# Kernel tuning notes

Hardware: AMD Instinct MI355X
Metric: run time of the kernel (lower is better)

Reference implementation:

```python
import jax, jax.numpy as jnp
from jax import lax
import numpy as np

TAU = 10.0      # tauSr == tauRef
THR = 1.0       # theta
WIDTH = 1.0     # tauRho (surrogate width)
SCALE = 1.0     # scaleRho (surrogate scale)
DECAY = float(np.exp(-1.0 / TAU))


@jax.custom_vjp
def _heaviside(v):
    # spike = 1[v >= theta]
    return (v >= THR).astype(v.dtype)

def _heaviside_fwd(v):
    return _heaviside(v), v

def _heaviside_bwd(v, g):
    # SLAYER exponential surrogate pdf: scaleRho/tauRho * exp(-|v-theta|/tauRho)
    return (g * (SCALE / WIDTH) * jnp.exp(-jnp.abs(v - THR) / WIDTH),)

_heaviside.defvjp(_heaviside_fwd, _heaviside_bwd)


def _conv2d(x, w, pad):
    # x: (B, Cin, H, W), w: (Cout, Cin, kh, kw); SLAYER convs have no bias
    return lax.conv_general_dilated(
        x, w, window_strides=(1, 1), padding=[(pad, pad), (pad, pad)],
        dimension_numbers=("NCHW", "OIHW", "NCHW"))


def _sumpool(x, k):
    # SLAYER pool = sum over kxk window (times a learned scalar applied outside)
    B, C, H, W = x.shape
    return x.reshape(B, C, H // k, k, W // k, k).sum(axis=(3, 5))


def _psp(seq):
    # exponential synaptic (PSP) filter along time: s[t] = a*s[t-1] + x[t]
    a = jnp.asarray(DECAY, seq.dtype)
    def step(s, x_t):
        s = a * s + x_t
        return s, s
    _, out = lax.scan(step, jnp.zeros_like(seq[0]), seq)
    return out  # (T, ...)


def _spikes(u):
    # thresholded spiking with decaying refractory feedback (scaleRef=1):
    # v[t] = u[t] - r[t]; s[t] = 1[v >= theta]; r[t+1] = b*(r[t] + theta*s[t])
    b = jnp.asarray(DECAY, u.dtype)
    def step(r, u_t):
        s = _heaviside(u_t - r)
        r_next = b * (r + THR * s)
        return r_next, s
    _, out = lax.scan(step, jnp.zeros_like(u[0]), u)
    return out  # (T, ...)


def _forward(x, conv1_w, conv2_w, lin_w, w_pool1, w_pool2):
    N, T, C, H, W = x.shape  # (64, 100, 2, 32, 32)
    h = _conv2d(x.reshape(N * T, C, H, W), conv1_w, 2)        # (NT, 4, 32, 32)
    h = _sumpool(h, 4) * w_pool1                               # (NT, 4, 8, 8)
    h = h.reshape(N, T, 4, 8, 8).swapaxes(0, 1)                # (T, N, 4, 8, 8)
    s1 = _spikes(_psp(h))                                      # (T, N, 4, 8, 8)
    h2 = _conv2d(s1.reshape(T * N, 4, 8, 8), conv2_w, 1)       # (TN, 8, 8, 8)
    h2 = (_sumpool(h2, 2) * w_pool2).reshape(T, N, 8, 4, 4)    # (T, N, 8, 4, 4)
    s2 = _spikes(_psp(h2))                                     # (T, N, 8, 4, 4)
    # dense = full-spatial conv (2, 8, 4, 4) -> (N, T, 2)
    return jnp.einsum("tnchw,ochw->nto", s2, lin_w)


def setup_inputs() -> dict:
    key = jax.random.key(0)
    ks = jax.random.split(key, 4)
    x = (jax.random.uniform(ks[0], (64, 100, 2, 32, 32)) < 0.1).astype(jnp.float32)
    conv1_w = jax.random.normal(ks[1], (4, 2, 5, 5), jnp.float32) * 0.3
    conv2_w = jax.random.normal(ks[2], (8, 4, 3, 3), jnp.float32) * 0.3
    lin_w = jax.random.normal(ks[3], (2, 8, 4, 4), jnp.float32) * 0.3
    w_pool1 = jnp.float32(1.0 / 16.0)  # 1.1*theta / (16 * 1.1)
    w_pool2 = jnp.float32(1.0 / 4.0)   # 1.1*theta / (4 * 1.1)
    return {"x": x, "conv1_w": conv1_w, "conv2_w": conv2_w, "lin_w": lin_w,
            "w_pool1": w_pool1, "w_pool2": w_pool2}


def reference(x, conv1_w, conv2_w, lin_w, w_pool1, w_pool2):
    return _forward(x, conv1_w, conv2_w, lin_w, w_pool1, w_pool2)
```

## Files before the change

### kernel.cpp

```cpp
#include <hip/hip_runtime.h>


#define DECAY 0.9048374180359595f

#define BAR_LGKM() asm volatile("s_waitcnt lgkmcnt(0)\n\ts_barrier" ::: "memory")
#define FENCE_LGKM() asm volatile("s_waitcnt lgkmcnt(0)" ::: "memory")

__global__ __launch_bounds__(128) void k0_fold(const float* __restrict__ w1,
        const float* __restrict__ w2, const float* __restrict__ wp1,
        const float* __restrict__ wp2, float* __restrict__ wl1,
        float* __restrict__ wl2, float* __restrict__ out) {
    const int tid = threadIdx.x;
    out[blockIdx.x * 128 + tid] = 0.f;
    if (blockIdx.x != 0) return;
    const float p1 = wp1[0], p2 = wp2[0];
    for (int idx = tid; idx < 512; idx += 128) {
        const int f = idx & 7, c = (idx >> 3) & 3, e = (idx >> 5) & 7, cin = idx >> 8;
        const int cc = c * 2 + cin;
        int alo = e - 3; if (alo < 0) alo = 0;
        int ahi = e;     if (ahi > 4) ahi = 4;
        int blo = f - 3; if (blo < 0) blo = 0;
        int bhi = f;     if (bhi > 4) bhi = 4;
        float s = 0.f;
        for (int a = alo; a <= ahi; ++a)
            for (int b = blo; b <= bhi; ++b)
                s += w1[cc * 25 + a * 5 + b];
        wl1[(cin * 8 + e) * 32 + c * 8 + f] = s * p1;
    }
    for (int idx = tid; idx < 512; idx += 128) {
        const int c2 = idx & 7, f = (idx >> 3) & 3, e = (idx >> 5) & 3, cin = idx >> 7;
        int alo = e - 1; if (alo < 0) alo = 0;
        int ahi = e;     if (ahi > 2) ahi = 2;
        int blo = f - 1; if (blo < 0) blo = 0;
        int bhi = f;     if (bhi > 2) bhi = 2;
        float s = 0.f;
        for (int aa = alo; aa <= ahi; ++aa)
            for (int bb = blo; bb <= bhi; ++bb)
                s += w2[((c2 * 4 + cin) * 3 + aa) * 3 + bb];
        wl2[c2 * 68 + cin * 16 + e * 4 + f] = s * p2;
    }
}

__global__ __launch_bounds__(64) void k1(const float* __restrict__ x,
        const float* __restrict__ wg, float* __restrict__ u1) {
    __shared__ __align__(16) float xs[2 * 1296];
    __shared__ __align__(16) float wl[512];
    const int lane = threadIdx.x;
    const int frame = blockIdx.x;
    const int n = frame / 100, t = frame % 100;

    *(float4*)(wl + 4 * lane)       = *(const float4*)(wg + 4 * lane);
    *(float4*)(wl + 256 + 4 * lane) = *(const float4*)(wg + 256 + 4 * lane);

    #pragma unroll
    for (int m0 = 0; m0 < 128; m0 += 64) {
        const int m = m0 + lane;
        if (m < 72) {
            const int cin = m / 36, rem = m % 36;
            const int rr = rem / 9, q4 = rem % 9;
            const int pr = (rr == 0) ? 0 : (rr == 1) ? 9 : (rr == 2) ? 26 : 35;
            *(float4*)(xs + cin * 1296 + pr * 36 + q4 * 4) = make_float4(0.f, 0.f, 0.f, 0.f);
        }
    }
    #pragma unroll
    for (int m0 = 0; m0 < 192; m0 += 64) {
        const int m = m0 + lane;
        if (m < 144) {
            const int cin = m / 72, rem = m % 72;
            const int side = rem & 1, pr = rem >> 1;
            *(float2*)(xs + cin * 1296 + pr * 36 + side * 34) = make_float2(0.f, 0.f);
        }
    }
    const float4* xg = (const float4*)(x + (size_t)frame * 2048);
    #pragma unroll
    for (int q = 0; q < 8; ++q) {
        const int m = q * 64 + lane;
        const float4 v = xg[m];
        const int li = 4 * m;
        const int cin = li >> 10, row = (li >> 5) & 31, col = li & 31;
        const int r = row + 2;
        const int pr = (r & 3) * 9 + (r >> 2);
        float* d = xs + cin * 1296 + pr * 36 + col + 2;
        *(float2*)(d)     = make_float2(v.x, v.y);
        *(float2*)(d + 2) = make_float2(v.z, v.w);
    }
    FENCE_LGKM();

    const int cp = lane >> 5;
    const int i  = (lane >> 2) & 7;
    const int jh = (lane >> 1) & 1;
    const int eh = lane & 1;

    float acc[2][4] = {{0.f, 0.f, 0.f, 0.f}, {0.f, 0.f, 0.f, 0.f}};
    const float* tb = xs + (i + eh) * 36 + jh * 16;
    #pragma unroll
    for (int cin = 0; cin < 2; ++cin) {
        #pragma unroll
        for (int et = 0; et < 4; ++et) {
            const int ro = cin * 1296 + et * 9 * 36;
            float xr[20];
            #pragma unroll
            for (int b = 0; b < 5; ++b)
                *(float4*)(xr + 4 * b) = *(const float4*)(tb + ro + 4 * b);
            float wv[16];
            const float* wp = wl + (cin * 8 + eh * 4 + et) * 32 + cp * 16;
            #pragma unroll
            for (int q = 0; q < 4; ++q)
                *(float4*)(wv + 4 * q) = *(const float4*)(wp + 4 * q);
            #pragma unroll
            for (int cl = 0; cl < 2; ++cl) {
                #pragma unroll
                for (int jj = 0; jj < 4; ++jj) {
                    const int o = 4 * jj;
                    acc[cl][jj] += xr[o]*wv[cl*8]     + xr[o+1]*wv[cl*8+1]
                                 + xr[o+2]*wv[cl*8+2] + xr[o+3]*wv[cl*8+3]
                                 + xr[o+4]*wv[cl*8+4] + xr[o+5]*wv[cl*8+5]
                                 + xr[o+6]*wv[cl*8+6] + xr[o+7]*wv[cl*8+7];
                }
            }
        }
    }
    #pragma unroll
    for (int cl = 0; cl < 2; ++cl)
        #pragma unroll
        for (int jj = 0; jj < 4; ++jj)
            acc[cl][jj] += __shfl_xor(acc[cl][jj], 1);

    const float o0 = eh ? acc[1][0] : acc[0][0];
    const float o1 = eh ? acc[1][1] : acc[0][1];
    const float o2 = eh ? acc[1][2] : acc[0][2];
    const float o3 = eh ? acc[1][3] : acc[0][3];
    *(float4*)(u1 + (size_t)t * 16384 + n * 256 + (2 * cp + eh) * 64 + i * 8 + jh * 4) =
        make_float4(o0, o1, o2, o3);
}

__global__ __launch_bounds__(256) void kf(const float* __restrict__ u1,
        const float* __restrict__ wl2g, const float* __restrict__ lw,
        float* __restrict__ out) {
    __shared__ __align__(16) float ls1[32 * 660];
    __shared__ __align__(16) float ls2[32 * 36];
    const int tid = threadIdx.x;
    const int n = blockIdx.x >> 2, qtr = blockIdx.x & 3;
    const int wave = tid >> 6, l64 = tid & 63;
    const float a = DECAY;

    for (int m = tid; m < 5280; m += 256)
        *(float4*)(ls1 + 4 * m) = make_float4(0.f, 0.f, 0.f, 0.f);

    const int cs = tid >> 6, rowi = (tid >> 3) & 7, col = tid & 7;
    const int pr1 = (((rowi + 1) & 1) * 5) + ((rowi + 1) >> 1);
    const int woff = cs * 160 + pr1 * 16 + 1 + col;
    const float* up = u1 + n * 256 + tid;

    const int sub = tid >> 4, l16 = tid & 15;
    const int c2l = l16 >> 3, i2 = (l16 >> 1) & 3, jhp = l16 & 1;
    const int c2g = qtr * 2 + c2l;

    float4 wreg[16];
    {
        const float* wbase = wl2g + c2g * 68;
        #pragma unroll
        for (int q = 0; q < 16; ++q)
            wreg[q] = *(const float4*)(wbase + (q >> 2) * 16 + (q & 3) * 4);
    }

    float dwA[8], dwB[8];
    {
        const int idx = l64 & 3;
        #pragma unroll
        for (int m = 0; m < 8; ++m) {
            dwA[m] = lw[qtr * 32 + idx * 8 + m];
            dwB[m] = lw[128 + qtr * 32 + idx * 8 + m];
        }
    }

    float psp = 0.f, rr = 0.f;
    float psp2 = 0.f, rr2 = 0.f;

    float vbuf[32];
    #pragma unroll
    for (int k = 0; k < 32; ++k) vbuf[k] = up[(size_t)k * 16384];

    BAR_LGKM();

    #pragma unroll 1
    for (int rd = 0; rd < 4; ++rd) {
        const int t0 = rd * 32;
        const int cnt = (rd == 3) ? 4 : 32;

        float sreg[32];
        #pragma unroll
        for (int k = 0; k < 32; ++k) {
            if (k < cnt) {
                psp = a * psp + vbuf[k];
                const float vv = psp - rr;
                const float s = (vv >= 1.f) ? 1.f : 0.f;
                rr = a * (rr + s);
                sreg[k] = s;
            }
        }
        #pragma unroll
        for (int k = 0; k < 32; ++k) {
            const int tt = t0 + 32 + k;
            if (tt < 100) vbuf[k] = up[(size_t)tt * 16384];
        }
        #pragma unroll
        for (int k = 0; k < 32; ++k)
            if (k < cnt) ls1[k * 660 + woff] = sreg[k];
        BAR_LGKM();

        #pragma unroll
        for (int pass = 0; pass < 2; ++pass) {
            const int slot = sub + 16 * pass;
            if (slot < cnt) {
                const float* tb = ls1 + slot * 660 + i2 * 16 + 4 * jhp;
                float acc0 = 0.f, acc1 = 0.f;
                #pragma unroll
                for (int cin = 0; cin < 4; ++cin) {
                    #pragma unroll
                    for (int e = 0; e < 4; ++e) {
                        const int C = cin * 160 + ((e & 1) * 5 + (e >> 1)) * 16;
                        float xr[6];
                        *(float4*)(xr)     = *(const float4*)(tb + C);
                        *(float2*)(xr + 4) = *(const float2*)(tb + C + 4);
                        const float4 wf = wreg[cin * 4 + e];
                        acc0 += xr[0] * wf.x; acc0 += xr[1] * wf.y;
                        acc0 += xr[2] * wf.z; acc0 += xr[3] * wf.w;
                        acc1 += xr[2] * wf.x; acc1 += xr[3] * wf.y;
                        acc1 += xr[4] * wf.z; acc1 += xr[5] * wf.w;
                    }
                }
                *(float2*)(ls2 + slot * 36 + c2l * 16 + i2 * 4 + 2 * jhp) =
                    make_float2(acc0, acc1);
            }
        }
        BAR_LGKM();

        if (wave == 0) {
            if (l64 < 32) {
                #pragma unroll
                for (int k = 0; k < 32; ++k) {
                    if (k < cnt) {
                        const float u = ls2[k * 36 + l64];
                        psp2 = a * psp2 + u;
                        const float vv = psp2 - rr2;
                        const float s = (vv >= 1.f) ? 1.f : 0.f;
                        rr2 = a * (rr2 + s);
                        ls2[k * 36 + l64] = s;
                    }
                }
            }
            FENCE_LGKM();
            #pragma unroll
            for (int pass = 0; pass < 2; ++pass) {
                const int slot = (l64 >> 2) + 16 * pass;
                const int idx = l64 & 3;
                if (slot < cnt) {
                    float a0 = 0.f, a1 = 0.f;
                    #pragma unroll
                    for (int m = 0; m < 8; ++m) {
                        const float s = ls2[slot * 36 + idx * 8 + m];
                        a0 += s * dwA[m];
                        a1 += s * dwB[m];
                    }
                    a0 += __shfl_down(a0, 2); a0 += __shfl_down(a0, 1);
                    a1 += __shfl_down(a1, 2); a1 += __shfl_down(a1, 1);
                    if (idx == 0) {
                        const int tt = t0 + slot;
                        atomicAdd(&out[n * 200 + tt * 2],     a0);
                        atomicAdd(&out[n * 200 + tt * 2 + 1], a1);
                    }
                }
            }
        }
    }
}

extern "C" void kernel_launch(void* const* d_in, const int* in_sizes, int n_in,
                              void* d_out, int out_size, void* d_ws, size_t ws_size,
                              hipStream_t stream) {
    const float* x   = (const float*)d_in[0];
    const float* w1  = (const float*)d_in[1];
    const float* w2  = (const float*)d_in[2];
    const float* lw  = (const float*)d_in[3];
    const float* wp1 = (const float*)d_in[4];
    const float* wp2 = (const float*)d_in[5];

    float* u1  = (float*)d_ws;
    float* wl1 = u1 + 1638400;
    float* wl2 = wl1 + 512;
    float* out = (float*)d_out;

    k0_fold<<<100, 128, 0, stream>>>(w1, w2, wp1, wp2, wl1, wl2, out);
    k1<<<6400, 64, 0, stream>>>(x, wl1, u1);
    kf<<<256, 256, 0, stream>>>(u1, wl2, lw, out);
}
```

Measured before the change: 123.9 us.

## Process all 100 timesteps in one pass with unpadded spike layout in LDS

The final fused kernel now loads all 100 timesteps of conv1 output into registers up front, runs the first spiking recurrence over the whole sequence, and stores spikes into a compact unpadded LDS buffer. The 4-round chunked pipeline and its per-round barriers are gone, and conv2 handles padding with clamped row indices and selects instead of a zero-padded halo layout. This removes the zero-initialisation pass and most barriers. In exchange it uses about 118 KB of LDS and 100 live registers per thread, which can cut occupancy or cause spills, and it no longer overlaps loads with compute across rounds.

Measured after the change: 119.8 us. 3.3% less time.

```diff
diff --git a/kernel.cpp b/kernel.cpp
--- a/kernel.cpp
+++ b/kernel.cpp
@@ -137,19 +137,13 @@
 __global__ __launch_bounds__(256) void kf(const float* __restrict__ u1,
         const float* __restrict__ wl2g, const float* __restrict__ lw,
         float* __restrict__ out) {
-    __shared__ __align__(16) float ls1[32 * 660];
-    __shared__ __align__(16) float ls2[32 * 36];
+    __shared__ __align__(16) float ls1[100 * 260];
+    __shared__ __align__(16) float ls2[100 * 36];
     const int tid = threadIdx.x;
     const int n = blockIdx.x >> 2, qtr = blockIdx.x & 3;
     const int wave = tid >> 6, l64 = tid & 63;
     const float a = DECAY;
 
-    for (int m = tid; m < 5280; m += 256)
-        *(float4*)(ls1 + 4 * m) = make_float4(0.f, 0.f, 0.f, 0.f);
-
-    const int cs = tid >> 6, rowi = (tid >> 3) & 7, col = tid & 7;
-    const int pr1 = (((rowi + 1) & 1) * 5) + ((rowi + 1) >> 1);
-    const int woff = cs * 160 + pr1 * 16 + 1 + col;
     const float* up = u1 + n * 256 + tid;
 
     const int sub = tid >> 4, l16 = tid & 15;
@@ -174,102 +168,94 @@
         }
     }
 
-    float psp = 0.f, rr = 0.f;
-    float psp2 = 0.f, rr2 = 0.f;
-
-    float vbuf[32];
-    #pragma unroll
-    for (int k = 0; k < 32; ++k) vbuf[k] = up[(size_t)k * 16384];
-
+    float vbuf[100];
+    #pragma unroll
+    for (int k = 0; k < 100; ++k) vbuf[k] = up[(size_t)k * 16384];
+    {
+        float psp = 0.f, rr = 0.f;
+        #pragma unroll
+        for (int k = 0; k < 100; ++k) {
+            psp = a * psp + vbuf[k];
+            const float vv = psp - rr;
+            const float s = (vv >= 1.f) ? 1.f : 0.f;
+            rr = a * (rr + s);
+            ls1[k * 260 + tid] = s;
+        }
+    }
     BAR_LGKM();
 
     #pragma unroll 1
-    for (int rd = 0; rd < 4; ++rd) {
-        const int t0 = rd * 32;
-        const int cnt = (rd == 3) ? 4 : 32;
-
-        float sreg[32];
-        #pragma unroll
-        for (int k = 0; k < 32; ++k) {
-            if (k < cnt) {
-                psp = a * psp + vbuf[k];
-                const float vv = psp - rr;
+    for (int pass = 0; pass < 7; ++pass) {
+        const int slot = sub + 16 * pass;
+        if (slot < 100) {
+            const float* sb = ls1 + slot * 260;
+            float acc0 = 0.f, acc1 = 0.f;
+            #pragma unroll
+            for (int cin = 0; cin < 4; ++cin) {
+                #pragma unroll
+                for (int e = 0; e < 4; ++e) {
+                    const int ri = 2 * i2 + e - 1;
+                    const int rc = (ri < 0) ? 0 : (ri > 7 ? 7 : ri);
+                    const bool rok = (ri >= 0) && (ri <= 7);
+                    float rr8[8];
+                    const float* rp = sb + cin * 64 + rc * 8;
+                    *(float4*)(rr8)     = *(const float4*)(rp);
+                    *(float4*)(rr8 + 4) = *(const float4*)(rp + 4);
+                    float xr[6];
+                    xr[0] = jhp ? rr8[3] : 0.0f;
+                    xr[1] = jhp ? rr8[4] : rr8[0];
+                    xr[2] = jhp ? rr8[5] : rr8[1];
+                    xr[3] = jhp ? rr8[6] : rr8[2];
+                    xr[4] = jhp ? rr8[7] : rr8[3];
+                    xr[5] = jhp ? 0.0f   : rr8[4];
+                    if (!rok) {
+                        #pragma unroll
+                        for (int m = 0; m < 6; ++m) xr[m] = 0.0f;
+                    }
+                    const float4 wf = wreg[cin * 4 + e];
+                    acc0 += xr[0] * wf.x; acc0 += xr[1] * wf.y;
+                    acc0 += xr[2] * wf.z; acc0 += xr[3] * wf.w;
+                    acc1 += xr[2] * wf.x; acc1 += xr[3] * wf.y;
+                    acc1 += xr[4] * wf.z; acc1 += xr[5] * wf.w;
+                }
+            }
+            *(float2*)(ls2 + slot * 36 + c2l * 16 + i2 * 4 + 2 * jhp) =
+                make_float2(acc0, acc1);
+        }
+    }
+    BAR_LGKM();
+
+    if (wave == 0) {
+        if (l64 < 32) {
+            float psp2 = 0.f, rr2 = 0.f;
+            #pragma unroll
+            for (int k = 0; k < 100; ++k) {
+                const float u = ls2[k * 36 + l64];
+                psp2 = a * psp2 + u;
+                const float vv = psp2 - rr2;
                 const float s = (vv >= 1.f) ? 1.f : 0.f;
-                rr = a * (rr + s);
-                sreg[k] = s;
-            }
-        }
-        #pragma unroll
-        for (int k = 0; k < 32; ++k) {
-            const int tt = t0 + 32 + k;
-            if (tt < 100) vbuf[k] = up[(size_t)tt * 16384];
-        }
-        #pragma unroll
-        for (int k = 0; k < 32; ++k)
-            if (k < cnt) ls1[k * 660 + woff] = sreg[k];
-        BAR_LGKM();
-
-        #pragma unroll
-        for (int pass = 0; pass < 2; ++pass) {
-            const int slot = sub + 16 * pass;
-            if (slot < cnt) {
-                const float* tb = ls1 + slot * 660 + i2 * 16 + 4 * jhp;
-                float acc0 = 0.f, acc1 = 0.f;
+                rr2 = a * (rr2 + s);
+                ls2[k * 36 + l64] = s;
+            }
+        }
+        FENCE_LGKM();
+        const int idx = l64 & 3;
+        #pragma unroll 1
+        for (int pass = 0; pass < 7; ++pass) {
+            const int slot = (l64 >> 2) + 16 * pass;
+            if (slot < 100) {
+                float a0 = 0.f, a1 = 0.f;
                 #pragma unroll
-                for (int cin = 0; cin < 4; ++cin) {
-                    #pragma unroll
-                    for (int e = 0; e < 4; ++e) {
-                        const int C = cin * 160 + ((e & 1) * 5 + (e >> 1)) * 16;
-                        float xr[6];
-                        *(float4*)(xr)     = *(const float4*)(tb + C);
-                        *(float2*)(xr + 4) = *(const float2*)(tb + C + 4);
-                        const float4 wf = wreg[cin * 4 + e];
-                        acc0 += xr[0] * wf.x; acc0 += xr[1] * wf.y;
-                        acc0 += xr[2] * wf.z; acc0 += xr[3] * wf.w;
-                        acc1 += xr[2] * wf.x; acc1 += xr[3] * wf.y;
-                        acc1 += xr[4] * wf.z; acc1 += xr[5] * wf.w;
-                    }
-                }
-                *(float2*)(ls2 + slot * 36 + c2l * 16 + i2 * 4 + 2 * jhp) =
-                    make_float2(acc0, acc1);
-            }
-        }
-        BAR_LGKM();
-
-        if (wave == 0) {
-            if (l64 < 32) {
-                #pragma unroll
-                for (int k = 0; k < 32; ++k) {
-                    if (k < cnt) {
-                        const float u = ls2[k * 36 + l64];
-                        psp2 = a * psp2 + u;
-                        const float vv = psp2 - rr2;
-                        const float s = (vv >= 1.f) ? 1.f : 0.f;
-                        rr2 = a * (rr2 + s);
-                        ls2[k * 36 + l64] = s;
-                    }
-                }
-            }
-            FENCE_LGKM();
-            #pragma unroll
-            for (int pass = 0; pass < 2; ++pass) {
-                const int slot = (l64 >> 2) + 16 * pass;
-                const int idx = l64 & 3;
-                if (slot < cnt) {
-                    float a0 = 0.f, a1 = 0.f;
-                    #pragma unroll
-                    for (int m = 0; m < 8; ++m) {
-                        const float s = ls2[slot * 36 + idx * 8 + m];
-                        a0 += s * dwA[m];
-                        a1 += s * dwB[m];
-                    }
-                    a0 += __shfl_down(a0, 2); a0 += __shfl_down(a0, 1);
-                    a1 += __shfl_down(a1, 2); a1 += __shfl_down(a1, 1);
-                    if (idx == 0) {
-                        const int tt = t0 + slot;
-                        atomicAdd(&out[n * 200 + tt * 2],     a0);
-                        atomicAdd(&out[n * 200 + tt * 2 + 1], a1);
-                    }
+                for (int m = 0; m < 8; ++m) {
+                    const float s = ls2[slot * 36 + idx * 8 + m];
+                    a0 += s * dwA[m];
+                    a1 += s * dwB[m];
+                }
+                a0 += __shfl_down(a0, 2); a0 += __shfl_down(a0, 1);
+                a1 += __shfl_down(a1, 2); a1 += __shfl_down(a1, 1);
+                if (idx == 0) {
+                    atomicAdd(&out[n * 200 + slot * 2],     a0);
+                    atomicAdd(&out[n * 200 + slot * 2 + 1], a1);
                 }
             }
         }
```
